# Optimization experiments

Measured on AMD Instinct MI355X. Metric: run time of the kernel, lower is better.

Reference implementation:

```python
import jax, jax.numpy as jnp
import numpy as np

H = 1024      # hidden_size
P = 32        # num_props -> output dim 2P=64
E = 8         # num_experts
C = 4         # num_centroids
K = 2         # top_k
B = 16384     # batch
TEMP = 0.1

def _glorot(key, shape):
    fan_in, fan_out = shape[-2], shape[-1]
    lim = jnp.sqrt(6.0 / (fan_in + fan_out))
    return jax.random.uniform(key, shape, jnp.float32, -lim, lim)

def setup_inputs() -> dict:
    key = jax.random.key(0)
    ks = jax.random.split(key, 16)
    return {
        'multimodal_feat': jax.random.normal(ks[0], (B, H), jnp.float32),
        'query_feat': jax.random.normal(ks[1], (B, H), jnp.float32),
        'ln_gamma': jnp.ones((H,), jnp.float32),
        'ln_beta': jnp.zeros((H,), jnp.float32),
        'pilot_emb': _glorot(ks[2], (E, C, H)),
        'qproj_W': _glorot(ks[3], (2 * H, H)),
        'qproj_b': jnp.zeros((H,), jnp.float32),
        'eW1': _glorot(ks[4], (E, H, H)),
        'eb1': jnp.zeros((E, H), jnp.float32),
        'eW2': _glorot(ks[5], (E, H, 2 * P)),
        'eb2': jnp.zeros((E, 2 * P), jnp.float32),
        'sW1': _glorot(ks[6], (H, H)),
        'sb1': jnp.zeros((H,), jnp.float32),
        'sW2': _glorot(ks[7], (H, 2 * P)),
        'sb2': jnp.zeros((2 * P,), jnp.float32),
        'gate_W': _glorot(ks[8], (4 * P, 2 * P)),
        'gate_b': jnp.zeros((2 * P,), jnp.float32),
    }

def _layer_norm(x, g, b, eps=1e-5):
    mu = jnp.mean(x, axis=-1, keepdims=True)
    var = jnp.var(x, axis=-1, keepdims=True)
    return (x - mu) * jax.lax.rsqrt(var + eps) * g + b

def _l2norm(x, axis=-1, eps=1e-12):
    n = jnp.linalg.norm(x, axis=axis, keepdims=True)
    return x / jnp.maximum(n, eps)

def reference(multimodal_feat, query_feat, ln_gamma, ln_beta, pilot_emb,
              qproj_W, qproj_b, eW1, eb1, eW2, eb2,
              sW1, sb1, sW2, sb2, gate_W, gate_b):
    bsz = multimodal_feat.shape[0]
    x = _layer_norm(multimodal_feat, ln_gamma, ln_beta)  # [B,H]

    # --- router ---
    fused = jnp.concatenate([x, query_feat], axis=-1)        # [B,2H]
    q = _l2norm(fused @ qproj_W + qproj_b)                   # [B,H]
    pilots = _l2norm(pilot_emb)                              # [E,C,H]
    sims = jnp.einsum('bh,ech->bec', q, pilots)              # [B,E,C]
    expert_scores = sims.mean(axis=-1)                       # [B,E]
    expert_probs = jax.nn.softmax(expert_scores / TEMP, axis=-1)
    topk_w, topk_idx = jax.lax.top_k(expert_probs, K)        # [B,K]
    topk_w = topk_w / (topk_w.sum(axis=-1, keepdims=True) + 1e-6)

    # combine weights per expert: [B,E]
    onehot = jax.nn.one_hot(topk_idx, E, dtype=x.dtype)      # [B,K,E]
    cw = jnp.einsum('bk,bke->be', topk_w, onehot)            # [B,E]

    # --- routed experts (dense all-expert compute, weighted combine) ---
    h = jax.nn.relu(jnp.einsum('bh,ehd->ebd', x, eW1) + eb1[:, None, :])  # [E,B,H]
    eout = jnp.einsum('ebd,edp->ebp', h, eW2) + eb2[:, None, :]           # [E,B,2P]
    routed = jnp.einsum('be,ebp->bp', cw, eout)                           # [B,2P]

    # --- shared expert + gate ---
    sh = jax.nn.relu(x @ sW1 + sb1)
    shared = sh @ sW2 + sb2                                   # [B,2P]
    combined = jnp.concatenate([routed, shared], axis=-1)     # [B,4P]
    out = combined @ gate_W + gate_b                          # [B,2P]

    gauss_params = jax.nn.sigmoid(out).reshape(bsz * P, 2)
    return gauss_params
```

## Files before the change

kernel.cpp:

```cpp
#include <hip/hip_runtime.h>
#include <hip/hip_bf16.h>
#include <stdint.h>

typedef unsigned short u16;
typedef __attribute__((ext_vector_type(8))) short short8;
typedef __attribute__((ext_vector_type(4))) float f32x4;

#define NB 16384
#define NH 1024
#define NSLOT 49152
#define NCHUNK 4

static __device__ __forceinline__ u16 f2bf(float f){
  union { float f; uint32_t u; } a; a.f = f;
  return (u16)((a.u + 0x7fffu + ((a.u >> 16) & 1u)) >> 16);
}

static __device__ __forceinline__ void gld16(const u16* gsrc, u16* lds){
  __builtin_amdgcn_global_load_lds((const __attribute__((address_space(1))) void*)gsrc,
                                   (__attribute__((address_space(3))) void*)lds, 16, 0, 0);
}

__global__ __launch_bounds__(256) void k_token_prep(
    const float* __restrict__ mm, const float* __restrict__ qf,
    const float* __restrict__ gamma, const float* __restrict__ beta,
    u16* __restrict__ fusedb, float* __restrict__ mu, float* __restrict__ rstd)
{
  int b = blockIdx.x, t = threadIdx.x;
  __shared__ float red[16];
  float4 v = ((const float4*)(mm + (size_t)b*NH))[t];
  float s = v.x+v.y+v.z+v.w;
  for (int o=32;o;o>>=1) s += __shfl_down(s,o);
  int wid = t>>6, lane = t&63;
  if (!lane) red[wid] = s;
  __syncthreads();
  if (t==0) red[8] = (red[0]+red[1]+red[2]+red[3]) * (1.0f/NH);
  __syncthreads();
  float mean = red[8];
  float4 d; d.x=v.x-mean; d.y=v.y-mean; d.z=v.z-mean; d.w=v.w-mean;
  float s2 = d.x*d.x+d.y*d.y+d.z*d.z+d.w*d.w;
  for (int o=32;o;o>>=1) s2 += __shfl_down(s2,o);
  if (!lane) red[4+wid] = s2;
  __syncthreads();
  if (t==0) red[9] = rsqrtf((red[4]+red[5]+red[6]+red[7])*(1.0f/NH) + 1e-5f);
  __syncthreads();
  float rs = red[9];
  if (t==0){ mu[b]=mean; rstd[b]=rs; }
  float4 g = ((const float4*)gamma)[t], be = ((const float4*)beta)[t];
  ushort4 ox;
  ox.x = f2bf(d.x*rs*g.x+be.x); ox.y = f2bf(d.y*rs*g.y+be.y);
  ox.z = f2bf(d.z*rs*g.z+be.z); ox.w = f2bf(d.w*rs*g.w+be.w);
  ((ushort4*)(fusedb + (size_t)b*2048))[t] = ox;
  float4 q = ((const float4*)(qf + (size_t)b*NH))[t];
  ushort4 oq; oq.x=f2bf(q.x); oq.y=f2bf(q.y); oq.z=f2bf(q.z); oq.w=f2bf(q.w);
  ((ushort4*)(fusedb + (size_t)b*2048 + 1024))[t] = oq;
}

__global__ __launch_bounds__(256) void k_pilots(const float* __restrict__ pe, float* __restrict__ pn)
{
  int ec = blockIdx.x, t = threadIdx.x;
  __shared__ double dred[8];
  float4 v = ((const float4*)(pe + (size_t)ec*NH))[t];
  double s2 = (double)v.x*v.x + (double)v.y*v.y + (double)v.z*v.z + (double)v.w*v.w;
  for (int o=32;o;o>>=1) s2 += __shfl_down(s2,o);
  int wid=t>>6, lane=t&63;
  if (!lane) dred[wid]=s2;
  __syncthreads();
  if (t==0) dred[4] = 1.0 / fmax(sqrt(dred[0]+dred[1]+dred[2]+dred[3]), 1e-12);
  __syncthreads();
  double inv = dred[4];
  float4 o; o.x=(float)(v.x*inv); o.y=(float)(v.y*inv); o.z=(float)(v.z*inv); o.w=(float)(v.w*inv);
  ((float4*)(pn + (size_t)ec*NH))[t] = o;
}

__global__ __launch_bounds__(256) void k_M(const float* __restrict__ W, const float* __restrict__ pn,
                                           double* __restrict__ M)
{
  int j = blockIdx.x;
  __shared__ float wrow[NH];
  __shared__ double part[256];
  for (int i=threadIdx.x;i<NH;i+=256) wrow[i] = W[(size_t)j*NH + i];
  __syncthreads();
  int ec = threadIdx.x>>3, seg = threadIdx.x&7;
  const float* p = pn + (size_t)ec*NH + seg*128;
  const float* wr = wrow + seg*128;
  double a = 0;
  #pragma unroll 8
  for (int i=0;i<128;i++) a += (double)wr[i]*(double)p[i];
  part[threadIdx.x] = a;
  __syncthreads();
  if (seg==0){
    double s=0;
    for (int i=0;i<8;i++) s += part[(ec<<3)+i];
    M[(size_t)j*32 + ec] = s;
  }
}

__global__ __launch_bounds__(256) void k_smalls(
    const float* eb1, const float* sb1, const float* eb2, const float* sb2,
    const float* gW, const float* gb, const float* qb, const float* pn,
    float* b1_all, float* cvec, double* cr)
{
  int idx = blockIdx.x*256 + threadIdx.x;
  if (idx < 9216){
    int e = idx>>10, k = idx&1023;
    b1_all[idx] = (e<8) ? eb1[idx] : sb1[k];
  } else if (idx < 9216+576){
    int i = idx-9216; int e = i>>6, n = i&63;
    float a = (e<8) ? 0.0f : gb[n];
    for (int j=0;j<64;j++){
      float bj = (e<8) ? eb2[e*64+j] : sb2[j];
      a += bj * gW[(((e<8)?j:64+j))*64 + n];
    }
    cvec[i] = a;
  } else if (idx < 9216+576+32){
    int ec = idx-9216-576;
    double a=0;
    for (int h=0;h<NH;h++) a += (double)qb[h]*(double)pn[(size_t)ec*NH+h];
    cr[ec] = a;
  }
}

__global__ __launch_bounds__(256) void k_transpose_bf16(const float* __restrict__ src, u16* __restrict__ dst,
                                                        int K, int N)
{
  __shared__ float tile[32][33];
  int k0 = blockIdx.x*32, n0 = blockIdx.y*32;
  int tx = threadIdx.x & 31, ty = threadIdx.x >> 5;
  for (int i=0;i<4;i++) tile[ty+i*8][tx] = src[(size_t)(k0+ty+i*8)*N + n0 + tx];
  __syncthreads();
  for (int i=0;i<4;i++) dst[(size_t)(n0+ty+i*8)*K + k0 + tx] = f2bf(tile[tx][ty+i*8]);
}

__global__ __launch_bounds__(256) void k_w1t(const float* __restrict__ eW1, const float* __restrict__ sW1,
                                             u16* __restrict__ w1t)
{
  __shared__ float tile[32][33];
  int e = blockIdx.z;
  const float* src = (e<8) ? eW1 + ((size_t)e<<20) : sW1;
  u16* dst = w1t + ((size_t)e<<20);
  int k0 = blockIdx.x*32, n0 = blockIdx.y*32;
  int tx = threadIdx.x & 31, ty = threadIdx.x >> 5;
  for (int i=0;i<4;i++) tile[ty+i*8][tx] = src[(size_t)(k0+ty+i*8)*NH + n0 + tx];
  __syncthreads();
  for (int i=0;i<4;i++) dst[(size_t)(n0+ty+i*8)*NH + k0 + tx] = f2bf(tile[tx][ty+i*8]);
}

__global__ __launch_bounds__(256) void k_fold_w2(const float* __restrict__ eW2, const float* __restrict__ sW2,
                                                 const float* __restrict__ gW, u16* __restrict__ w2t)
{
  __shared__ float gsh[64*64];
  int e = blockIdx.y;
  const float* src = (e<8) ? eW2 + (size_t)e*NH*64 : sW2;
  int rowbase = (e<8) ? 0 : 64;
  for (int i=threadIdx.x;i<64*64;i+=256) gsh[i] = gW[(size_t)(rowbase + (i>>6))*64 + (i&63)];
  __syncthreads();
  int flat = blockIdx.x*256 + threadIdx.x;
  int n = flat >> 10, k = flat & 1023;
  float acc = 0;
  #pragma unroll 8
  for (int j=0;j<64;j++) acc += src[(size_t)k*64 + j] * gsh[j*64 + n];
  w2t[(size_t)e*64*NH + flat] = f2bf(acc);
}

__global__ __launch_bounds__(256) void k_router(
    const float* __restrict__ mm, const float* __restrict__ qf,
    const float* __restrict__ gamma, const float* __restrict__ beta,
    const float* __restrict__ mu, const float* __restrict__ rstd,
    const double* __restrict__ M, double* __restrict__ u_part)
{
  __shared__ float At[16][130];
  __shared__ double Ms[16][32];
  int rb = blockIdx.x * 128;
  int kc = blockIdx.y * 512;
  bool isx = (kc < 1024);
  const float* src = isx ? mm : qf;
  int ksrc = isx ? kc : kc-1024;
  int t = threadIdx.x;
  int kk4 = (t&3)*4, rr = t>>2;
  int rg4 = t & 31, ec0 = (t>>5)*4;
  double acc[4][4] = {};

  for (int kb=0; kb<512; kb+=16){
    __syncthreads();
    float4 g4, b4;
    if (isx){ g4 = *(const float4*)(gamma + kc+kb+kk4); b4 = *(const float4*)(beta + kc+kb+kk4); }
    #pragma unroll
    for (int i=0;i<2;i++){
      int r = rr + i*64;
      float4 v = *(const float4*)(src + (size_t)(rb+r)*NH + ksrc + kb + kk4);
      if (isx){
        float m = mu[rb+r], rs = rstd[rb+r];
        v.x=(v.x-m)*rs*g4.x+b4.x; v.y=(v.y-m)*rs*g4.y+b4.y;
        v.z=(v.z-m)*rs*g4.z+b4.z; v.w=(v.w-m)*rs*g4.w+b4.w;
      }
      At[kk4+0][r]=v.x; At[kk4+1][r]=v.y; At[kk4+2][r]=v.z; At[kk4+3][r]=v.w;
    }
    const double* msrc = M + (size_t)(kc+kb)*32;
    ((double*)Ms)[t]     = msrc[t];
    ((double*)Ms)[256+t] = msrc[256+t];
    __syncthreads();
    #pragma unroll
    for (int kk=0; kk<16; kk++){
      float a4[4]; double m4[4];
      #pragma unroll
      for (int i=0;i<4;i++) a4[i] = At[kk][rg4 + 32*i];
      #pragma unroll
      for (int j=0;j<4;j++) m4[j] = Ms[kk][ec0+j];
      #pragma unroll
      for (int i=0;i<4;i++)
        #pragma unroll
        for (int j=0;j<4;j++) acc[i][j] = fma((double)a4[i], m4[j], acc[i][j]);
    }
  }
  double* dst = u_part + ((size_t)blockIdx.y*NB + rb)*32;
  #pragma unroll
  for (int i=0;i<4;i++){
    size_t row = (size_t)(rg4 + 32*i);
    #pragma unroll
    for (int j=0;j<4;j++) dst[row*32 + ec0 + j] = acc[i][j];
  }
}

__global__ __launch_bounds__(256,2) void k_qnorm(
    const u16* __restrict__ fusedb, const u16* __restrict__ wqt,
    const float* __restrict__ qb, float* __restrict__ norm2)
{
  __shared__ u16 As[128*32];
  __shared__ u16 Bs[128*32];
  int nb = blockIdx.x*128, mb = blockIdx.y*128;
  int t = threadIdx.x;
  int r0 = t>>2, c16 = (t&3)*8;
  const u16* ag0 = fusedb + (size_t)(mb+r0)*2048 + c16;
  const u16* ag1 = fusedb + (size_t)(mb+r0+64)*2048 + c16;
  const u16* bg0 = wqt + (size_t)(nb+r0)*2048 + c16;
  const u16* bg1 = wqt + (size_t)(nb+r0+64)*2048 + c16;
  u16* la0 = As + t*8;  u16* la1 = As + 2048 + t*8;
  u16* lb0 = Bs + t*8;  u16* lb1 = Bs + 2048 + t*8;
  int wid=t>>6, lane=t&63, quad=lane>>4, lr=lane&15;
  int wm=(wid&1)*64, wn=(wid>>1)*64;
  f32x4 acc[4][4] = {};
  for (int kb=0;kb<2048;kb+=32){
    __syncthreads();
    gld16(ag0+kb, la0); gld16(ag1+kb, la1);
    gld16(bg0+kb, lb0); gld16(bg1+kb, lb1);
    __syncthreads();
    short8 af[4], bf4[4];
    #pragma unroll
    for (int i=0;i<4;i++) af[i]  = *(const short8*)(As + (wm+i*16+lr)*32 + quad*8);
    #pragma unroll
    for (int j=0;j<4;j++) bf4[j] = *(const short8*)(Bs + (wn+j*16+lr)*32 + quad*8);
    #pragma unroll
    for (int i=0;i<4;i++)
      #pragma unroll
      for (int j=0;j<4;j++)
        acc[i][j] = __builtin_amdgcn_mfma_f32_16x16x32_bf16(af[i], bf4[j], acc[i][j], 0,0,0);
  }
  float rsum[4][4];
  #pragma unroll
  for (int i=0;i<4;i++)
    #pragma unroll
    for (int r=0;r<4;r++){
      float s=0;
      #pragma unroll
      for (int j=0;j<4;j++){
        int n = nb + wn + j*16 + lr;
        float v = acc[i][j][r] + qb[n];
        s += v*v;
      }
      rsum[i][r]=s;
    }
  #pragma unroll
  for (int m=1;m<16;m<<=1)
    #pragma unroll
    for (int i=0;i<4;i++)
      #pragma unroll
      for (int r=0;r<4;r++) rsum[i][r] += __shfl_xor(rsum[i][r], m);
  if (lr==0){
    #pragma unroll
    for (int i=0;i<4;i++)
      #pragma unroll
      for (int r=0;r<4;r++)
        unsafeAtomicAdd(&norm2[mb + wm + i*16 + quad*4 + r], rsum[i][r]);
  }
}

__global__ __launch_bounds__(256) void k_scores(
    const double* __restrict__ u_part, const double* __restrict__ cr, const float* __restrict__ norm2,
    int2* __restrict__ idx2, float2* __restrict__ w12, int* __restrict__ counts)
{
  __shared__ int lcnt[8];
  int t = threadIdx.x;
  if (t<8) lcnt[t]=0;
  __syncthreads();
  int b = blockIdx.x*256 + t;
  double s[8];
  #pragma unroll
  for (int e=0;e<8;e++) s[e] = cr[e*4]+cr[e*4+1]+cr[e*4+2]+cr[e*4+3];
  for (int c=0;c<NCHUNK;c++){
    const double* up = u_part + ((size_t)c*NB + b)*32;
    #pragma unroll
    for (int e=0;e<8;e++) s[e] += up[e*4]+up[e*4+1]+up[e*4+2]+up[e*4+3];
  }
  double inv = 0.25 / fmax(sqrt((double)norm2[b]), 1e-12);
  #pragma unroll
  for (int e=0;e<8;e++) s[e] *= inv;
  int e1 = 0;
  for (int e=1;e<8;e++) if (s[e] > s[e1]) e1 = e;
  int e2 = (e1==0) ? 1 : 0;
  for (int e=0;e<8;e++) if (e!=e1 && s[e] > s[e2]) e2 = e;
  double mx = s[e1], S = 0, p[8];
  #pragma unroll
  for (int e=0;e<8;e++){ p[e] = exp((s[e]-mx)*10.0); S += p[e]; }
  double P1 = p[e1]/S, P2 = p[e2]/S;
  double den = P1 + P2 + 1e-6;
  idx2[b] = make_int2(e1,e2);
  w12[b]  = make_float2((float)(P1/den), (float)(P2/den));
  atomicAdd(&lcnt[e1],1); atomicAdd(&lcnt[e2],1);
  __syncthreads();
  if (t<8) atomicAdd(&counts[t], lcnt[t]);
}

__global__ void k_prefix(const int* counts, int* offs, int* cursor){
  if (threadIdx.x==0 && blockIdx.x==0){
    int o=0;
    for (int e=0;e<8;e++){ offs[e]=o; cursor[e]=o; o+=counts[e]; }
    offs[8]=o;
  }
}

__global__ __launch_bounds__(256) void k_fill(const int2* __restrict__ idx2, const float2* __restrict__ w12,
                                              int* cursor, int* __restrict__ tok_list, float* __restrict__ wt_list)
{
  __shared__ int lc[8], base[8];
  int t = threadIdx.x;
  if (t<8) lc[t]=0;
  __syncthreads();
  int b = blockIdx.x*256 + t;
  int2 e = idx2[b]; float2 w = w12[b];
  int p1 = atomicAdd(&lc[e.x],1);
  int p2 = atomicAdd(&lc[e.y],1);
  __syncthreads();
  if (t<8) base[t] = atomicAdd(&cursor[t], lc[t]);
  __syncthreads();
  int s1 = base[e.x]+p1, s2 = base[e.y]+p2;
  tok_list[s1]=b; wt_list[s1]=w.x;
  tok_list[s2]=b; wt_list[s2]=w.y;
  tok_list[2*NB + b] = b; wt_list[2*NB + b] = 1.0f;
}

__global__ __launch_bounds__(256,2) void k_gemm1(
    const u16* __restrict__ fusedb, const u16* __restrict__ w1t, const float* __restrict__ b1_all,
    const int* __restrict__ tok_list, const int* __restrict__ offs, const int* __restrict__ counts,
    u16* __restrict__ h)
{
  int e = blockIdx.z;
  int cnt = (e<8) ? counts[e] : NB;
  int off = (e<8) ? offs[e]   : 2*NB;
  int mb = blockIdx.y * 128;
  if (mb >= cnt) return;
  int rem = cnt - mb;
  int nb = blockIdx.x * 128;
  __shared__ u16 As[128*32];
  __shared__ u16 Bs[128*32];
  int t = threadIdx.x;
  int r0 = t>>2, c16 = (t&3)*8;
  int r0c = r0    < rem ? r0    : rem-1;
  int r1c = r0+64 < rem ? r0+64 : rem-1;
  int tok0 = tok_list[off + mb + r0c];
  int tok1 = tok_list[off + mb + r1c];
  const u16* wbase = w1t + ((size_t)e<<20);
  const u16* ag0 = fusedb + (size_t)tok0*2048 + c16;
  const u16* ag1 = fusedb + (size_t)tok1*2048 + c16;
  const u16* bg0 = wbase + (size_t)(nb+r0)*NH + c16;
  const u16* bg1 = wbase + (size_t)(nb+r0+64)*NH + c16;
  u16* la0 = As + t*8;  u16* la1 = As + 2048 + t*8;
  u16* lb0 = Bs + t*8;  u16* lb1 = Bs + 2048 + t*8;
  int wid=t>>6, lane=t&63, quad=lane>>4, lr=lane&15;
  int wm=(wid&1)*64, wn=(wid>>1)*64;
  f32x4 acc[4][4] = {};
  for (int kb=0;kb<1024;kb+=32){
    __syncthreads();
    gld16(ag0+kb, la0); gld16(ag1+kb, la1);
    gld16(bg0+kb, lb0); gld16(bg1+kb, lb1);
    __syncthreads();
    short8 af[4], bf4[4];
    #pragma unroll
    for (int i=0;i<4;i++) af[i]  = *(const short8*)(As + (wm+i*16+lr)*32 + quad*8);
    #pragma unroll
    for (int j=0;j<4;j++) bf4[j] = *(const short8*)(Bs + (wn+j*16+lr)*32 + quad*8);
    #pragma unroll
    for (int i=0;i<4;i++)
      #pragma unroll
      for (int j=0;j<4;j++)
        acc[i][j] = __builtin_amdgcn_mfma_f32_16x16x32_bf16(af[i], bf4[j], acc[i][j], 0,0,0);
  }
  const float* b1 = b1_all + e*NH;
  #pragma unroll
  for (int i=0;i<4;i++){
    #pragma unroll
    for (int reg=0; reg<4; reg++){
      int rr = wm + i*16 + quad*4 + reg;
      if (rr < rem){
        size_t hrow = (size_t)(off + mb + rr) * NH;
        #pragma unroll
        for (int j=0;j<4;j++){
          int n = nb + wn + j*16 + lr;
          float v = acc[i][j][reg] + b1[n];
          h[hrow + n] = f2bf(fmaxf(v, 0.0f));
        }
      }
    }
  }
}

__global__ __launch_bounds__(256,2) void k_gemm2(
    const u16* __restrict__ h, const u16* __restrict__ w2t,
    const int* __restrict__ tok_list, const float* __restrict__ wt_list,
    const int* __restrict__ offs, const int* __restrict__ counts,
    float* __restrict__ out_acc)
{
  int e = blockIdx.y;
  int cnt = (e<8) ? counts[e] : NB;
  int off = (e<8) ? offs[e]   : 2*NB;
  int mb = blockIdx.x * 128;
  if (mb >= cnt) return;
  int rem = cnt - mb;
  __shared__ u16 As[128*32];
  __shared__ u16 Bs[64*32];
  int t = threadIdx.x;
  int r0 = t>>2, c16 = (t&3)*8;
  const u16* ah = h + (size_t)(off+mb)*NH;
  const u16* ag0 = ah + (size_t)r0*NH + c16;
  const u16* ag1 = ah + (size_t)(r0+64)*NH + c16;
  const u16* bg0 = w2t + (size_t)e*64*NH + (size_t)r0*NH + c16;
  u16* la0 = As + t*8;  u16* la1 = As + 2048 + t*8;
  u16* lb0 = Bs + t*8;
  int wid=t>>6, lane=t&63, quad=lane>>4, lr=lane&15;
  int wm = wid*32;
  f32x4 acc[2][4] = {};
  for (int kb=0;kb<1024;kb+=32){
    __syncthreads();
    gld16(ag0+kb, la0); gld16(ag1+kb, la1);
    gld16(bg0+kb, lb0);
    __syncthreads();
    short8 af[2], bf4[4];
    #pragma unroll
    for (int i=0;i<2;i++) af[i]  = *(const short8*)(As + (wm+i*16+lr)*32 + quad*8);
    #pragma unroll
    for (int j=0;j<4;j++) bf4[j] = *(const short8*)(Bs + (j*16+lr)*32 + quad*8);
    #pragma unroll
    for (int i=0;i<2;i++)
      #pragma unroll
      for (int j=0;j<4;j++)
        acc[i][j] = __builtin_amdgcn_mfma_f32_16x16x32_bf16(af[i], bf4[j], acc[i][j], 0,0,0);
  }
  #pragma unroll
  for (int i=0;i<2;i++){
    #pragma unroll
    for (int reg=0; reg<4; reg++){
      int rr = wm + i*16 + quad*4 + reg;
      if (rr < rem){
        int slot = off + mb + rr;
        int tok = tok_list[slot];
        float w = wt_list[slot];
        float* dst = out_acc + (size_t)tok*64;
        #pragma unroll
        for (int j=0;j<4;j++)
          unsafeAtomicAdd(dst + j*16 + lr, w * acc[i][j][reg]);
      }
    }
  }
}

__global__ __launch_bounds__(256) void k_final(
    const float* __restrict__ out_acc, const float* __restrict__ cvec,
    const int2* __restrict__ idx2, const float2* __restrict__ w12, float* __restrict__ out)
{
  int i = blockIdx.x*256 + threadIdx.x;
  int b = i>>6, n = i&63;
  int2 e = idx2[b]; float2 w = w12[b];
  float v = out_acc[i] + w.x*cvec[e.x*64+n] + w.y*cvec[e.y*64+n] + cvec[8*64+n];
  out[i] = 1.0f / (1.0f + expf(-v));
}

extern "C" void kernel_launch(void* const* d_in, const int* in_sizes, int n_in,
                              void* d_out, int out_size, void* d_ws, size_t ws_size,
                              hipStream_t stream)
{
  (void)in_sizes; (void)n_in; (void)out_size; (void)ws_size;
  const float* mm   =(const float*)d_in[0];
  const float* qf   =(const float*)d_in[1];
  const float* gamma=(const float*)d_in[2];
  const float* beta =(const float*)d_in[3];
  const float* pe   =(const float*)d_in[4];
  const float* qW   =(const float*)d_in[5];
  const float* qb   =(const float*)d_in[6];
  const float* eW1  =(const float*)d_in[7];
  const float* eb1  =(const float*)d_in[8];
  const float* eW2  =(const float*)d_in[9];
  const float* eb2  =(const float*)d_in[10];
  const float* sW1  =(const float*)d_in[11];
  const float* sb1  =(const float*)d_in[12];
  const float* sW2  =(const float*)d_in[13];
  const float* sb2  =(const float*)d_in[14];
  const float* gW   =(const float*)d_in[15];
  const float* gb   =(const float*)d_in[16];
  float* out = (float*)d_out;

  char* p = (char*)d_ws;
  auto alloc = [&](size_t bytes)->char*{ char* r = p; p += (bytes + 255) & ~(size_t)255; return r; };
  float*  out_acc = (float*) alloc((size_t)NB*64*4);
  float*  norm2   = (float*) alloc((size_t)NB*4);
  int*    counts  = (int*)   alloc(64);
  int*    cursor  = (int*)   alloc(64);
  int*    offs    = (int*)   alloc(64);
  size_t zero_bytes = (size_t)(p - (char*)d_ws);
  double* u_part  = (double*)alloc((size_t)NCHUNK*NB*32*8);
  u16*    fusedb  = (u16*)   alloc((size_t)NB*2048*2);
  u16*    h       = (u16*)   alloc((size_t)NSLOT*NH*2);
  u16*    w1t     = (u16*)   alloc((size_t)9*NH*NH*2);
  u16*    wqt     = (u16*)   alloc((size_t)NH*2048*2);
  u16*    w2t     = (u16*)   alloc((size_t)9*64*NH*2);
  float*  b1_all  = (float*) alloc((size_t)9*NH*4);
  float*  cvec    = (float*) alloc((size_t)9*64*4);
  double* M       = (double*)alloc((size_t)2048*32*8);
  float*  pn      = (float*) alloc((size_t)32*NH*4);
  double* cr      = (double*)alloc(32*8);
  float*  mu      = (float*) alloc((size_t)NB*4);
  float*  rstd    = (float*) alloc((size_t)NB*4);
  int2*   idx2    = (int2*)  alloc((size_t)NB*8);
  float2* w12     = (float2*)alloc((size_t)NB*8);
  int*    tok_list= (int*)   alloc((size_t)NSLOT*4);
  float*  wt_list = (float*) alloc((size_t)NSLOT*4);

  hipMemsetAsync(d_ws, 0, zero_bytes, stream);
  k_token_prep<<<NB, 256, 0, stream>>>(mm, qf, gamma, beta, fusedb, mu, rstd);
  k_pilots<<<32, 256, 0, stream>>>(pe, pn);
  k_M<<<2048, 256, 0, stream>>>(qW, pn, M);
  k_smalls<<<39, 256, 0, stream>>>(eb1, sb1, eb2, sb2, gW, gb, qb, pn, b1_all, cvec, cr);
  k_transpose_bf16<<<dim3(64,32), 256, 0, stream>>>(qW, wqt, 2048, 1024);
  k_w1t<<<dim3(32,32,9), 256, 0, stream>>>(eW1, sW1, w1t);
  k_fold_w2<<<dim3(256,9), 256, 0, stream>>>(eW2, sW2, gW, w2t);
  k_qnorm<<<dim3(8,128), 256, 0, stream>>>(fusedb, wqt, qb, norm2);
  k_router<<<dim3(128,NCHUNK), 256, 0, stream>>>(mm, qf, gamma, beta, mu, rstd, M, u_part);
  k_scores<<<64, 256, 0, stream>>>(u_part, cr, norm2, idx2, w12, counts);
  k_prefix<<<1, 64, 0, stream>>>(counts, offs, cursor);
  k_fill<<<64, 256, 0, stream>>>(idx2, w12, cursor, tok_list, wt_list);
  k_gemm1<<<dim3(8,128,9), 256, 0, stream>>>(fusedb, w1t, b1_all, tok_list, offs, counts, h);
  k_gemm2<<<dim3(128,9), 256, 0, stream>>>(h, w2t, tok_list, wt_list, offs, counts, out_acc);
  k_final<<<4096, 256, 0, stream>>>(out_acc, cvec, idx2, w12, out);
}
```

Before: 703.5 us.

## Fuse expert GEMM1 and GEMM2 via LDS hidden tiles, widen N-tile to 256

```diff
diff --git a/kernel.cpp b/kernel.cpp
--- a/kernel.cpp
+++ b/kernel.cpp
@@ -226,36 +226,39 @@
     const u16* __restrict__ fusedb, const u16* __restrict__ wqt,
     const float* __restrict__ qb, float* __restrict__ norm2)
 {
-  __shared__ u16 As[128*32];
-  __shared__ u16 Bs[128*32];
-  int nb = blockIdx.x*128, mb = blockIdx.y*128;
+  __shared__ __align__(16) u16 As[128*32];
+  __shared__ __align__(16) u16 Bs[256*32];
+  int nb = blockIdx.x*256, mb = blockIdx.y*128;
   int t = threadIdx.x;
   int r0 = t>>2, c16 = (t&3)*8;
   const u16* ag0 = fusedb + (size_t)(mb+r0)*2048 + c16;
   const u16* ag1 = fusedb + (size_t)(mb+r0+64)*2048 + c16;
   const u16* bg0 = wqt + (size_t)(nb+r0)*2048 + c16;
-  const u16* bg1 = wqt + (size_t)(nb+r0+64)*2048 + c16;
-  u16* la0 = As + t*8;  u16* la1 = As + 2048 + t*8;
-  u16* lb0 = Bs + t*8;  u16* lb1 = Bs + 2048 + t*8;
   int wid=t>>6, lane=t&63, quad=lane>>4, lr=lane&15;
-  int wm=(wid&1)*64, wn=(wid>>1)*64;
-  f32x4 acc[4][4] = {};
+  int wm=(wid&1)*64, wn=(wid>>1)*128;
+  f32x4 acc[4][8] = {};
   for (int kb=0;kb<2048;kb+=32){
     __syncthreads();
-    gld16(ag0+kb, la0); gld16(ag1+kb, la1);
-    gld16(bg0+kb, lb0); gld16(bg1+kb, lb1);
-    __syncthreads();
-    short8 af[4], bf4[4];
-    #pragma unroll
-    for (int i=0;i<4;i++) af[i]  = *(const short8*)(As + (wm+i*16+lr)*32 + quad*8);
-    #pragma unroll
-    for (int j=0;j<4;j++) bf4[j] = *(const short8*)(Bs + (wn+j*16+lr)*32 + quad*8);
+    gld16(ag0+kb, As + t*8); gld16(ag1+kb, As + 2048 + t*8);
+    gld16(bg0+kb,          Bs + t*8);
+    gld16(bg0+kb +  64*2048, Bs + 2048 + t*8);
+    gld16(bg0+kb + 128*2048, Bs + 4096 + t*8);
+    gld16(bg0+kb + 192*2048, Bs + 6144 + t*8);
+    __syncthreads();
+    short8 af[4], bf[8];
+    #pragma unroll
+    for (int i=0;i<4;i++) af[i] = *(const short8*)(As + (wm+i*16+lr)*32 + quad*8);
+    #pragma unroll
+    for (int j=0;j<8;j++) bf[j] = *(const short8*)(Bs + (wn+j*16+lr)*32 + quad*8);
     #pragma unroll
     for (int i=0;i<4;i++)
       #pragma unroll
-      for (int j=0;j<4;j++)
-        acc[i][j] = __builtin_amdgcn_mfma_f32_16x16x32_bf16(af[i], bf4[j], acc[i][j], 0,0,0);
-  }
+      for (int j=0;j<8;j++)
+        acc[i][j] = __builtin_amdgcn_mfma_f32_16x16x32_bf16(af[i], bf[j], acc[i][j], 0,0,0);
+  }
+  float qbv[8];
+  #pragma unroll
+  for (int j=0;j<8;j++) qbv[j] = qb[nb + wn + j*16 + lr];
   float rsum[4][4];
   #pragma unroll
   for (int i=0;i<4;i++)
@@ -263,9 +266,8 @@
     for (int r=0;r<4;r++){
       float s=0;
       #pragma unroll
-      for (int j=0;j<4;j++){
-        int n = nb + wn + j*16 + lr;
-        float v = acc[i][j][r] + qb[n];
+      for (int j=0;j<8;j++){
+        float v = acc[i][j][r] + qbv[j];
         s += v*v;
       }
       rsum[i][r]=s;
@@ -349,10 +351,12 @@
   tok_list[2*NB + b] = b; wt_list[2*NB + b] = 1.0f;
 }
 
-__global__ __launch_bounds__(256,2) void k_gemm1(
+__global__ __launch_bounds__(256,2) void k_expert(
     const u16* __restrict__ fusedb, const u16* __restrict__ w1t, const float* __restrict__ b1_all,
-    const int* __restrict__ tok_list, const int* __restrict__ offs, const int* __restrict__ counts,
-    u16* __restrict__ h)
+    const u16* __restrict__ w2t,
+    const int* __restrict__ tok_list, const float* __restrict__ wt_list,
+    const int* __restrict__ offs, const int* __restrict__ counts,
+    float* __restrict__ out_acc)
 {
   int e = blockIdx.z;
   int cnt = (e<8) ? counts[e] : NB;
@@ -360,10 +364,23 @@
   int mb = blockIdx.y * 128;
   if (mb >= cnt) return;
   int rem = cnt - mb;
-  int nb = blockIdx.x * 128;
-  __shared__ u16 As[128*32];
-  __shared__ u16 Bs[128*32];
+  int nb = blockIdx.x * 256;
+  __shared__ __align__(16) u16 As[128*32];
+  __shared__ __align__(16) u16 Bs[256*32];
+  __shared__ __align__(16) u16 B2[64*264];
+  __shared__ __align__(16) u16 hl[128*72];
   int t = threadIdx.x;
+
+  {
+    const u16* wb2 = w2t + (size_t)e*64*NH + nb;
+    #pragma unroll
+    for (int s=0;s<8;s++){
+      int flat = s*256 + t;
+      int row = flat>>5, c8 = (flat&31)*8;
+      *(uint4*)(B2 + row*264 + c8) = *(const uint4*)(wb2 + (size_t)row*NH + c8);
+    }
+  }
+
   int r0 = t>>2, c16 = (t&3)*8;
   int r0c = r0    < rem ? r0    : rem-1;
   int r1c = r0+64 < rem ? r0+64 : rem-1;
@@ -373,104 +390,83 @@
   const u16* ag0 = fusedb + (size_t)tok0*2048 + c16;
   const u16* ag1 = fusedb + (size_t)tok1*2048 + c16;
   const u16* bg0 = wbase + (size_t)(nb+r0)*NH + c16;
-  const u16* bg1 = wbase + (size_t)(nb+r0+64)*NH + c16;
-  u16* la0 = As + t*8;  u16* la1 = As + 2048 + t*8;
-  u16* lb0 = Bs + t*8;  u16* lb1 = Bs + 2048 + t*8;
   int wid=t>>6, lane=t&63, quad=lane>>4, lr=lane&15;
-  int wm=(wid&1)*64, wn=(wid>>1)*64;
-  f32x4 acc[4][4] = {};
+  int wm=(wid&1)*64, wn=(wid>>1)*128;
+  f32x4 acc[4][8] = {};
   for (int kb=0;kb<1024;kb+=32){
     __syncthreads();
-    gld16(ag0+kb, la0); gld16(ag1+kb, la1);
-    gld16(bg0+kb, lb0); gld16(bg1+kb, lb1);
-    __syncthreads();
-    short8 af[4], bf4[4];
-    #pragma unroll
-    for (int i=0;i<4;i++) af[i]  = *(const short8*)(As + (wm+i*16+lr)*32 + quad*8);
-    #pragma unroll
-    for (int j=0;j<4;j++) bf4[j] = *(const short8*)(Bs + (wn+j*16+lr)*32 + quad*8);
+    gld16(ag0+kb, As + t*8); gld16(ag1+kb, As + 2048 + t*8);
+    gld16(bg0+kb,           Bs + t*8);
+    gld16(bg0+kb +  64*NH,  Bs + 2048 + t*8);
+    gld16(bg0+kb + 128*NH,  Bs + 4096 + t*8);
+    gld16(bg0+kb + 192*NH,  Bs + 6144 + t*8);
+    __syncthreads();
+    short8 af[4], bf[8];
+    #pragma unroll
+    for (int i=0;i<4;i++) af[i] = *(const short8*)(As + (wm+i*16+lr)*32 + quad*8);
+    #pragma unroll
+    for (int j=0;j<8;j++) bf[j] = *(const short8*)(Bs + (wn+j*16+lr)*32 + quad*8);
     #pragma unroll
     for (int i=0;i<4;i++)
       #pragma unroll
-      for (int j=0;j<4;j++)
-        acc[i][j] = __builtin_amdgcn_mfma_f32_16x16x32_bf16(af[i], bf4[j], acc[i][j], 0,0,0);
-  }
-  const float* b1 = b1_all + e*NH;
-  #pragma unroll
-  for (int i=0;i<4;i++){
-    #pragma unroll
-    for (int reg=0; reg<4; reg++){
-      int rr = wm + i*16 + quad*4 + reg;
-      if (rr < rem){
-        size_t hrow = (size_t)(off + mb + rr) * NH;
+      for (int j=0;j<8;j++)
+        acc[i][j] = __builtin_amdgcn_mfma_f32_16x16x32_bf16(af[i], bf[j], acc[i][j], 0,0,0);
+  }
+
+  float b1v[8];
+  #pragma unroll
+  for (int j=0;j<8;j++) b1v[j] = b1_all[e*NH + nb + wn + j*16 + lr];
+
+  f32x4 acc2[2][4] = {};
+  int myhalf = wn>>7;
+  #pragma unroll
+  for (int jj=0;jj<4;jj++){
+    __syncthreads();
+    if ((jj>>1) == myhalf){
+      int j0 = (jj&1)*4;
+      #pragma unroll
+      for (int i=0;i<4;i++)
         #pragma unroll
-        for (int j=0;j<4;j++){
-          int n = nb + wn + j*16 + lr;
-          float v = acc[i][j][reg] + b1[n];
-          h[hrow + n] = f2bf(fmaxf(v, 0.0f));
-        }
-      }
-    }
-  }
-}
-
-__global__ __launch_bounds__(256,2) void k_gemm2(
-    const u16* __restrict__ h, const u16* __restrict__ w2t,
-    const int* __restrict__ tok_list, const float* __restrict__ wt_list,
-    const int* __restrict__ offs, const int* __restrict__ counts,
-    float* __restrict__ out_acc)
-{
-  int e = blockIdx.y;
-  int cnt = (e<8) ? counts[e] : NB;
-  int off = (e<8) ? offs[e]   : 2*NB;
-  int mb = blockIdx.x * 128;
-  if (mb >= cnt) return;
-  int rem = cnt - mb;
-  __shared__ u16 As[128*32];
-  __shared__ u16 Bs[64*32];
-  int t = threadIdx.x;
-  int r0 = t>>2, c16 = (t&3)*8;
-  const u16* ah = h + (size_t)(off+mb)*NH;
-  const u16* ag0 = ah + (size_t)r0*NH + c16;
-  const u16* ag1 = ah + (size_t)(r0+64)*NH + c16;
-  const u16* bg0 = w2t + (size_t)e*64*NH + (size_t)r0*NH + c16;
-  u16* la0 = As + t*8;  u16* la1 = As + 2048 + t*8;
-  u16* lb0 = Bs + t*8;
-  int wid=t>>6, lane=t&63, quad=lane>>4, lr=lane&15;
-  int wm = wid*32;
-  f32x4 acc[2][4] = {};
-  for (int kb=0;kb<1024;kb+=32){
-    __syncthreads();
-    gld16(ag0+kb, la0); gld16(ag1+kb, la1);
-    gld16(bg0+kb, lb0);
-    __syncthreads();
-    short8 af[2], bf4[4];
-    #pragma unroll
-    for (int i=0;i<2;i++) af[i]  = *(const short8*)(As + (wm+i*16+lr)*32 + quad*8);
-    #pragma unroll
-    for (int j=0;j<4;j++) bf4[j] = *(const short8*)(Bs + (j*16+lr)*32 + quad*8);
-    #pragma unroll
-    for (int i=0;i<2;i++)
-      #pragma unroll
-      for (int j=0;j<4;j++)
-        acc[i][j] = __builtin_amdgcn_mfma_f32_16x16x32_bf16(af[i], bf4[j], acc[i][j], 0,0,0);
-  }
-  #pragma unroll
-  for (int i=0;i<2;i++){
-    #pragma unroll
-    for (int reg=0; reg<4; reg++){
-      int rr = wm + i*16 + quad*4 + reg;
-      if (rr < rem){
-        int slot = off + mb + rr;
+        for (int j2=0;j2<4;j2++)
+          #pragma unroll
+          for (int reg=0;reg<4;reg++){
+            float v = acc[i][j0+j2][reg] + b1v[j0+j2];
+            hl[(wm+i*16+quad*4+reg)*72 + j2*16 + lr] = f2bf(fmaxf(v,0.0f));
+          }
+    }
+    __syncthreads();
+    #pragma unroll
+    for (int kk=0;kk<2;kk++){
+      short8 a2[2], b2f[4];
+      #pragma unroll
+      for (int i2=0;i2<2;i2++)
+        a2[i2] = *(const short8*)(hl + (wid*32+i2*16+lr)*72 + kk*32 + quad*8);
+      #pragma unroll
+      for (int j2=0;j2<4;j2++)
+        b2f[j2] = *(const short8*)(B2 + (j2*16+lr)*264 + jj*64 + kk*32 + quad*8);
+      #pragma unroll
+      for (int i2=0;i2<2;i2++)
+        #pragma unroll
+        for (int j2=0;j2<4;j2++)
+          acc2[i2][j2] = __builtin_amdgcn_mfma_f32_16x16x32_bf16(a2[i2], b2f[j2], acc2[i2][j2], 0,0,0);
+    }
+  }
+
+  #pragma unroll
+  for (int i2=0;i2<2;i2++)
+    #pragma unroll
+    for (int reg=0;reg<4;reg++){
+      int m = wid*32 + i2*16 + quad*4 + reg;
+      if (m < rem){
+        int slot = off + mb + m;
         int tok = tok_list[slot];
         float w = wt_list[slot];
         float* dst = out_acc + (size_t)tok*64;
         #pragma unroll
-        for (int j=0;j<4;j++)
-          unsafeAtomicAdd(dst + j*16 + lr, w * acc[i][j][reg]);
+        for (int j2=0;j2<4;j2++)
+          unsafeAtomicAdd(dst + j2*16 + lr, w * acc2[i2][j2][reg]);
       }
     }
-  }
 }
 
 __global__ __launch_bounds__(256) void k_final(
@@ -518,7 +514,6 @@
   size_t zero_bytes = (size_t)(p - (char*)d_ws);
   double* u_part  = (double*)alloc((size_t)NCHUNK*NB*32*8);
   u16*    fusedb  = (u16*)   alloc((size_t)NB*2048*2);
-  u16*    h       = (u16*)   alloc((size_t)NSLOT*NH*2);
   u16*    w1t     = (u16*)   alloc((size_t)9*NH*NH*2);
   u16*    wqt     = (u16*)   alloc((size_t)NH*2048*2);
   u16*    w2t     = (u16*)   alloc((size_t)9*64*NH*2);
@@ -542,12 +537,11 @@
   k_transpose_bf16<<<dim3(64,32), 256, 0, stream>>>(qW, wqt, 2048, 1024);
   k_w1t<<<dim3(32,32,9), 256, 0, stream>>>(eW1, sW1, w1t);
   k_fold_w2<<<dim3(256,9), 256, 0, stream>>>(eW2, sW2, gW, w2t);
-  k_qnorm<<<dim3(8,128), 256, 0, stream>>>(fusedb, wqt, qb, norm2);
+  k_qnorm<<<dim3(4,128), 256, 0, stream>>>(fusedb, wqt, qb, norm2);
   k_router<<<dim3(128,NCHUNK), 256, 0, stream>>>(mm, qf, gamma, beta, mu, rstd, M, u_part);
   k_scores<<<64, 256, 0, stream>>>(u_part, cr, norm2, idx2, w12, counts);
   k_prefix<<<1, 64, 0, stream>>>(counts, offs, cursor);
   k_fill<<<64, 256, 0, stream>>>(idx2, w12, cursor, tok_list, wt_list);
-  k_gemm1<<<dim3(8,128,9), 256, 0, stream>>>(fusedb, w1t, b1_all, tok_list, offs, counts, h);
-  k_gemm2<<<dim3(128,9), 256, 0, stream>>>(h, w2t, tok_list, wt_list, offs, counts, out_acc);
+  k_expert<<<dim3(4,128,9), 256, 0, stream>>>(fusedb, w1t, b1_all, w2t, tok_list, wt_list, offs, counts, out_acc);
   k_final<<<4096, 256, 0, stream>>>(out_acc, cvec, idx2, w12, out);
 }
```

Measured after the change: 660.9 us. -6.1%, faster.
